# Kernel tuning notes

Measured on AMD Instinct MI355X. Metric: run time of the kernel, lower is better.

The kernel has to match this reference:

```python
import jax, jax.numpy as jnp
import numpy as np

B, T, D, H = 4, 8192, 512, 512


def log_g(x):
    # log of the 'continuous relu-ish' gate: log(relu(x)+0.5) for x>=0, -softplus(-x) otherwise
    return jnp.where(x >= 0, jnp.log(jax.nn.relu(x) + 0.5), -jax.nn.softplus(-x))


def setup_inputs() -> dict:
    key = jax.random.key(0)
    ks = jax.random.split(key, 8)
    s = 1.0 / np.sqrt(D)
    return {
        "x": jax.random.normal(ks[0], (B, T, D), dtype=jnp.float32),
        "h_0": jax.random.normal(ks[1], (B, 1, H), dtype=jnp.float32),
        "W_f": jax.random.normal(ks[2], (D, H), dtype=jnp.float32) * s,
        "b_f": jnp.zeros((H,), dtype=jnp.float32),
        "W_i": jax.random.normal(ks[3], (D, H), dtype=jnp.float32) * s,
        "b_i": jnp.zeros((H,), dtype=jnp.float32),
        "W_h": jax.random.normal(ks[4], (D, H), dtype=jnp.float32) * s,
        "b_h": jnp.zeros((H,), dtype=jnp.float32),
    }


def reference(x, h_0, W_f, b_f, W_i, b_i, W_h, b_h):
    # three dense gate projections: [B,T,H]
    f_pre = jnp.einsum("btd,dh->bth", x, W_f) + b_f
    i_pre = jnp.einsum("btd,dh->bth", x, W_i) + b_i
    h_pre = jnp.einsum("btd,dh->bth", x, W_h) + b_h

    diff = jax.nn.softplus(-f_pre) - jax.nn.softplus(-i_pre)
    log_f = -jax.nn.softplus(diff)            # log forget gate  [B,T,H]
    log_i = -jax.nn.softplus(-diff)           # log input  gate  [B,T,H]

    log_h0 = log_g(h_0)                       # [B,1,H]
    log_tilde_h = log_g(h_pre)                # [B,T,H]
    log_values = jnp.concatenate([log_h0, log_i + log_tilde_h], axis=1)  # [B,T+1,H]

    # a_star[t] = sum_{s<=t} log_f[s], with a leading zero for the h_0 slot
    a_star = jnp.pad(jnp.cumsum(log_f, axis=1), ((0, 0), (1, 0), (0, 0)))  # [B,T+1,H]
    # stable parallel scan in log space
    log_h = a_star + jax.lax.cumlogsumexp(log_values - a_star, axis=1)     # [B,T+1,H]
    return jnp.exp(log_h)
```

## Files before the change

### kernel.cpp

```cpp
#include <hip/hip_runtime.h>
#include <hip/hip_bf16.h>

#define B_ 4
#define T_ 8192
#define D_ 512
#define H_ 512
#define M_ (B_ * T_)
#define CHUNK_ 128
#define SUB_ 32
#define NSUB_ (T_ / SUB_)
#define SEQS_ (B_ * H_)

typedef __attribute__((ext_vector_type(8))) short bf16x8;
typedef __attribute__((ext_vector_type(4))) float f32x4;

__device__ __forceinline__ unsigned short f2bf(float x) {
  union { float f; unsigned int u; } c; c.f = x;
  unsigned int u = c.u;
  unsigned int r = (u + 0x7fffu + ((u >> 16) & 1u)) >> 16;
  return (unsigned short)r;
}
__device__ __forceinline__ float bf2f(unsigned short h) {
  union { unsigned int u; float f; } c; c.u = ((unsigned int)h) << 16;
  return c.f;
}

__device__ __forceinline__ void gll16(const void* g, void* l) {
  __builtin_amdgcn_global_load_lds(
      (const __attribute__((address_space(1))) unsigned int*)g,
      (__attribute__((address_space(3))) unsigned int*)l, 16, 0, 0);
}

__global__ void convert_all(const float* __restrict__ x, const float* __restrict__ Wf,
                            const float* __restrict__ Wi, const float* __restrict__ Wh,
                            unsigned short* __restrict__ xbf, unsigned short* __restrict__ Wt) {
  const int gid = blockIdx.x * 256 + threadIdx.x;
  const size_t i = (size_t)gid * 4;
  const float4 a = *(const float4*)(x + i);
  ushort4 hv;
  hv.x = f2bf(a.x); hv.y = f2bf(a.y); hv.z = f2bf(a.z); hv.w = f2bf(a.w);
  *(ushort4*)(xbf + i) = hv;
  if (gid < 3 * H_ * D_ / 4) {
    const int g = gid >> 16;
    const int rem = gid & 65535;
    const int n = rem >> 7;
    const int k4 = (rem & 127) * 4;
    const float* W = (g == 0) ? Wf : (g == 1) ? Wi : Wh;
    ushort4 o;
    o.x = f2bf(W[(k4 + 0) * H_ + n]);
    o.y = f2bf(W[(k4 + 1) * H_ + n]);
    o.z = f2bf(W[(k4 + 2) * H_ + n]);
    o.w = f2bf(W[(k4 + 3) * H_ + n]);
    *(ushort4*)(Wt + ((size_t)g * H_ + n) * D_ + k4) = o;
  }
}

__global__ __launch_bounds__(256, 2)
void gemm_gates(const unsigned short* __restrict__ xb, const unsigned short* __restrict__ Wt,
                const float* __restrict__ bF, const float* __restrict__ bI,
                const float* __restrict__ bH, unsigned int* __restrict__ AV) {
  __shared__ unsigned short xs[128 * 64];
  __shared__ unsigned short wsm[3 * 64 * 64];

  const int tid = threadIdx.x;
  const int hb = blockIdx.x;
  const int m0 = blockIdx.y * 128;
  const int n0 = hb * 64;
  const int wave = tid >> 6;
  const int lane = tid & 63;
  const int wm = (wave & 1) * 64;
  const int wn = (wave >> 1) * 32;
  const int l16 = lane & 15;
  const int quad = lane >> 4;
  const int lrow = lane >> 3;
  const int lch = (lane & 7) ^ lrow;

  int xoff[4];
  #pragma unroll
  for (int j = 0; j < 4; ++j)
    xoff[j] = (m0 + (wave * 4 + j) * 8 + lrow) * D_ + lch * 8;
  int woff[6], wdst[6];
  #pragma unroll
  for (int q = 0; q < 6; ++q) {
    const int gw = wave * 6 + q;
    const int g = gw >> 3, rg = gw & 7;
    woff[q] = (g * H_ + n0 + rg * 8 + lrow) * D_ + lch * 8;
    wdst[q] = g * 4096 + rg * 512;
  }

  f32x4 acc[3][4][2];
  #pragma unroll
  for (int g = 0; g < 3; ++g)
    #pragma unroll
    for (int mi = 0; mi < 4; ++mi)
      #pragma unroll
      for (int ni = 0; ni < 2; ++ni)
        acc[g][mi][ni] = (f32x4){0.f, 0.f, 0.f, 0.f};

  #pragma unroll 1
  for (int kb = 0; kb < D_; kb += 64) {
    #pragma unroll
    for (int j = 0; j < 4; ++j)
      gll16(xb + xoff[j] + kb, xs + (wave * 4 + j) * 512);
    #pragma unroll
    for (int q = 0; q < 6; ++q)
      gll16(Wt + woff[q] + kb, wsm + wdst[q]);
    __syncthreads();

    #pragma unroll
    for (int kk = 0; kk < 64; kk += 32) {
      const int kc = kk >> 3;
      bf16x8 af[4];
      #pragma unroll
      for (int mi = 0; mi < 4; ++mi) {
        const int r = wm + mi * 16 + l16;
        af[mi] = *(const bf16x8*)(xs + r * 64 + ((kc + quad) ^ (r & 7)) * 8);
      }
      bf16x8 bfr[3][2];
      #pragma unroll
      for (int g = 0; g < 3; ++g)
        #pragma unroll
        for (int ni = 0; ni < 2; ++ni) {
          const int r = wn + ni * 16 + l16;
          bfr[g][ni] = *(const bf16x8*)(wsm + g * 4096 + r * 64 + ((kc + quad) ^ (r & 7)) * 8);
        }
      #pragma unroll
      for (int g = 0; g < 3; ++g)
        #pragma unroll
        for (int mi = 0; mi < 4; ++mi)
          #pragma unroll
          for (int ni = 0; ni < 2; ++ni)
            acc[g][mi][ni] = __builtin_amdgcn_mfma_f32_16x16x32_bf16(
                af[mi], bfr[g][ni], acc[g][mi][ni], 0, 0, 0);
    }
    __syncthreads();
  }

  const size_t avbase = ((size_t)blockIdx.y * 8 + hb) * (CHUNK_ * 64);
  #pragma unroll
  for (int ni = 0; ni < 2; ++ni) {
    const int hl = wn + ni * 16 + l16;
    const int col = n0 + hl;
    const float bfv = bF[col], biv = bI[col], bhv = bH[col];
    #pragma unroll
    for (int mi = 0; mi < 4; ++mi) {
      const int tb = wm + mi * 16 + quad * 4;
      #pragma unroll
      for (int r = 0; r < 4; ++r) {
        float fp = acc[0][mi][ni][r] + bfv;
        float ip = acc[1][mi][ni][r] + biv;
        float hp = acc[2][mi][ni][r] + bhv;
        fp = fminf(fmaxf(fp, -30.f), 30.f);
        ip = fminf(fmaxf(ip, -30.f), 30.f);
        hp = fminf(fmaxf(hp, -30.f), 30.f);
        const float Ef = __expf(-fp);
        const float Ei = __expf(-ip);
        const float rr2 = 1.f / (2.f + Ef + Ei);
        const float fgate = (1.f + Ei) * rr2;
        const float igate = (1.f + Ef) * rr2;
        float gval;
        if (hp >= 0.f) gval = hp + 0.5f;
        else gval = 1.f / (1.f + __expf(-hp));
        const float vval = igate * gval;
        AV[avbase + (size_t)(tb + r) * 64 + hl] =
            (unsigned int)f2bf(fgate) | ((unsigned int)f2bf(vval) << 16);
      }
    }
  }
}

__global__ void scan_pass1(const unsigned int* __restrict__ AV,
                           float* __restrict__ Fc, float* __restrict__ Sc) {
  const int gid = blockIdx.x * 256 + threadIdx.x;
  const int hl = gid & 63;
  const int rest = gid >> 6;
  const int hbi = rest & 7;
  const int sub = (rest >> 3) & 3;
  const int c = (rest >> 5) & 63;
  const int b = rest >> 11;
  const unsigned int* p = AV + (size_t)((b * 64 + c) * 8 + hbi) * (CHUNK_ * 64)
                             + sub * SUB_ * 64 + hl;
  float F = 1.f, S = 0.f;
  #pragma unroll 8
  for (int t = 0; t < SUB_; ++t) {
    const unsigned int w = p[t * 64];
    const float a = bf2f((unsigned short)(w & 0xffffu));
    const float v = bf2f((unsigned short)(w >> 16));
    F *= a;
    S = fmaf(a, S, v);
  }
  const int sidx = c * 4 + sub;
  const int seq = b * 512 + hbi * 64 + hl;
  Fc[(size_t)sidx * SEQS_ + seq] = F;
  Sc[(size_t)sidx * SEQS_ + seq] = S;
}

__global__ __launch_bounds__(256, 2)
void scan_pass2(const float* __restrict__ h0, const float* __restrict__ Fc,
                const float* __restrict__ Sc, float* __restrict__ Hin,
                float* __restrict__ out) {
  __shared__ float Fs[NSUB_ * 32];
  __shared__ float Ss[NSUB_ * 32];
  __shared__ float Fg[8 * 32], Sg[8 * 32], Hg[8 * 32];

  const int tid = threadIdx.x;
  const int seq0 = blockIdx.x * 32;

  #pragma unroll 8
  for (int i = tid; i < NSUB_ * 32; i += 256) {
    const int sub = i >> 5;
    const int sl = i & 31;
    Fs[i] = Fc[(size_t)sub * SEQS_ + seq0 + sl];
    Ss[i] = Sc[(size_t)sub * SEQS_ + seq0 + sl];
  }
  __syncthreads();

  const int g = tid >> 5;
  const int sl = tid & 31;
  {
    float F = 1.f, S = 0.f;
    #pragma unroll 8
    for (int j = 0; j < 32; ++j) {
      const int idx = (g * 32 + j) * 32 + sl;
      S = fmaf(Fs[idx], S, Ss[idx]);
      F *= Fs[idx];
    }
    Fg[g * 32 + sl] = F;
    Sg[g * 32 + sl] = S;
  }
  __syncthreads();

  if (tid < 32) {
    const int seq = seq0 + tid;
    const int b = seq >> 9;
    const int h = seq & 511;
    const float xv = h0[seq];
    float hcur = (xv >= 0.f) ? (xv + 0.5f) : (1.f / (1.f + __expf(-xv)));
    out[(size_t)(b * (T_ + 1)) * H_ + h] = hcur;
    #pragma unroll
    for (int gg = 0; gg < 8; ++gg) {
      Hg[gg * 32 + tid] = hcur;
      hcur = fmaf(Fg[gg * 32 + tid], hcur, Sg[gg * 32 + tid]);
    }
  }
  __syncthreads();

  float h = Hg[g * 32 + sl];
  #pragma unroll 8
  for (int j = 0; j < 32; ++j) {
    const int sub = g * 32 + j;
    const int idx = sub * 32 + sl;
    Hin[(size_t)sub * SEQS_ + seq0 + sl] = h;
    h = fmaf(Fs[idx], h, Ss[idx]);
  }
}

__global__ void scan_pass3(const unsigned int* __restrict__ AV,
                           const float* __restrict__ Hin, float* __restrict__ out) {
  const int gid = blockIdx.x * 256 + threadIdx.x;
  const int hl = gid & 63;
  const int rest = gid >> 6;
  const int hbi = rest & 7;
  const int sub = (rest >> 3) & 3;
  const int c = (rest >> 5) & 63;
  const int b = rest >> 11;
  const unsigned int* p = AV + (size_t)((b * 64 + c) * 8 + hbi) * (CHUNK_ * 64)
                             + sub * SUB_ * 64 + hl;
  float* o = out + ((size_t)(b * (T_ + 1) + c * CHUNK_ + sub * SUB_ + 1) * H_)
                 + hbi * 64 + hl;
  const int seq = b * 512 + hbi * 64 + hl;
  float hcur = Hin[(size_t)(c * 4 + sub) * SEQS_ + seq];
  #pragma unroll 8
  for (int t = 0; t < SUB_; ++t) {
    const unsigned int w = p[t * 64];
    const float a = bf2f((unsigned short)(w & 0xffffu));
    const float v = bf2f((unsigned short)(w >> 16));
    hcur = fmaf(a, hcur, v);
    o[(size_t)t * H_] = hcur;
  }
}

extern "C" void kernel_launch(void* const* d_in, const int* in_sizes, int n_in,
                              void* d_out, int out_size, void* d_ws, size_t ws_size,
                              hipStream_t stream) {
  const float* x  = (const float*)d_in[0];
  const float* h0 = (const float*)d_in[1];
  const float* Wf = (const float*)d_in[2];
  const float* bF = (const float*)d_in[3];
  const float* Wi = (const float*)d_in[4];
  const float* bI = (const float*)d_in[5];
  const float* Wh = (const float*)d_in[6];
  const float* bH = (const float*)d_in[7];
  float* out = (float*)d_out;

  char* ws = (char*)d_ws;
  size_t off = 0;
  unsigned int* AV = (unsigned int*)(ws + off);      off += (size_t)M_ * H_ * 4;
  unsigned short* xbf = (unsigned short*)(ws + off); off += (size_t)M_ * D_ * 2;
  unsigned short* Wt = (unsigned short*)(ws + off);  off += (size_t)3 * H_ * D_ * 2;
  float* Fc  = (float*)(ws + off); off += (size_t)NSUB_ * SEQS_ * 4;
  float* Sc  = (float*)(ws + off); off += (size_t)NSUB_ * SEQS_ * 4;
  float* Hin = (float*)(ws + off); off += (size_t)NSUB_ * SEQS_ * 4;

  convert_all<<<(M_ * D_ / 4) / 256, 256, 0, stream>>>(x, Wf, Wi, Wh, xbf, Wt);
  gemm_gates<<<dim3(H_ / 64, M_ / 128), 256, 0, stream>>>(xbf, Wt, bF, bI, bH, AV);
  scan_pass1<<<(SEQS_ * NSUB_) / 256, 256, 0, stream>>>(AV, Fc, Sc);
  scan_pass2<<<SEQS_ / 32, 256, 0, stream>>>(h0, Fc, Sc, Hin, out);
  scan_pass3<<<(SEQS_ * NSUB_) / 256, 256, 0, stream>>>(AV, Hin, out);
}
```

Before: 229.8 us.

## Fuse scan pass1 sub-chunk reduction into GEMM epilogue and remap blocks per XCD

The per-32-step sub-chunk scan summaries (product of forget gates and accumulated value) are now computed in the GEMM epilogue from the rounded bf16 gate values. Each lane combines its 4 rows and merges across quads with xor-shuffles, which removes the separate scan_pass1 kernel and its full re-read of the AV buffer. The grid is also flattened to 1D and remapped so that the eight H-blocks sharing one M-chunk land on the same XCD, aiming for better L2 reuse of x tiles. The cost is extra epilogue work and register pressure in the GEMM.

```diff
diff --git a/kernel.cpp b/kernel.cpp
--- a/kernel.cpp
+++ b/kernel.cpp
@@ -58,14 +58,20 @@
 __global__ __launch_bounds__(256, 2)
 void gemm_gates(const unsigned short* __restrict__ xb, const unsigned short* __restrict__ Wt,
                 const float* __restrict__ bF, const float* __restrict__ bI,
-                const float* __restrict__ bH, unsigned int* __restrict__ AV) {
+                const float* __restrict__ bH, unsigned int* __restrict__ AV,
+                float* __restrict__ Fc, float* __restrict__ Sc) {
   __shared__ unsigned short xs[128 * 64];
   __shared__ unsigned short wsm[3 * 64 * 64];
 
   const int tid = threadIdx.x;
-  const int hb = blockIdx.x;
-  const int m0 = blockIdx.y * 128;
+  const int bid = blockIdx.x;
+  const int xcd = bid & 7;
+  const int kseq = bid >> 3;
+  const int mc = (kseq & ~7) | xcd;
+  const int hb = kseq & 7;
+  const int m0 = mc * CHUNK_;
   const int n0 = hb * 64;
+
   const int wave = tid >> 6;
   const int lane = tid & 63;
   const int wm = (wave & 1) * 64;
@@ -136,15 +142,18 @@
     __syncthreads();
   }
 
-  const size_t avbase = ((size_t)blockIdx.y * 8 + hb) * (CHUNK_ * 64);
+  const size_t avbase = ((size_t)mc * 8 + hb) * (CHUNK_ * 64);
+  const int bb = mc >> 6, cc = mc & 63;
   #pragma unroll
   for (int ni = 0; ni < 2; ++ni) {
     const int hl = wn + ni * 16 + l16;
     const int col = n0 + hl;
     const float bfv = bF[col], biv = bI[col], bhv = bH[col];
+    float Fseg[4], Sseg[4];
     #pragma unroll
     for (int mi = 0; mi < 4; ++mi) {
       const int tb = wm + mi * 16 + quad * 4;
+      float Fs_ = 1.f, Ss_ = 0.f;
       #pragma unroll
       for (int r = 0; r < 4; ++r) {
         float fp = acc[0][mi][ni][r] + bfv;
@@ -162,37 +171,42 @@
         if (hp >= 0.f) gval = hp + 0.5f;
         else gval = 1.f / (1.f + __expf(-hp));
         const float vval = igate * gval;
+        const unsigned short ab = f2bf(fgate);
+        const unsigned short vb = f2bf(vval);
         AV[avbase + (size_t)(tb + r) * 64 + hl] =
-            (unsigned int)f2bf(fgate) | ((unsigned int)f2bf(vval) << 16);
+            (unsigned int)ab | ((unsigned int)vb << 16);
+        const float ar = bf2f(ab), vr = bf2f(vb);
+        Ss_ = fmaf(ar, Ss_, vr);
+        Fs_ *= ar;
       }
-    }
-  }
-}
-
-__global__ void scan_pass1(const unsigned int* __restrict__ AV,
-                           float* __restrict__ Fc, float* __restrict__ Sc) {
-  const int gid = blockIdx.x * 256 + threadIdx.x;
-  const int hl = gid & 63;
-  const int rest = gid >> 6;
-  const int hbi = rest & 7;
-  const int sub = (rest >> 3) & 3;
-  const int c = (rest >> 5) & 63;
-  const int b = rest >> 11;
-  const unsigned int* p = AV + (size_t)((b * 64 + c) * 8 + hbi) * (CHUNK_ * 64)
-                             + sub * SUB_ * 64 + hl;
-  float F = 1.f, S = 0.f;
-  #pragma unroll 8
-  for (int t = 0; t < SUB_; ++t) {
-    const unsigned int w = p[t * 64];
-    const float a = bf2f((unsigned short)(w & 0xffffu));
-    const float v = bf2f((unsigned short)(w >> 16));
-    F *= a;
-    S = fmaf(a, S, v);
-  }
-  const int sidx = c * 4 + sub;
-  const int seq = b * 512 + hbi * 64 + hl;
-  Fc[(size_t)sidx * SEQS_ + seq] = F;
-  Sc[(size_t)sidx * SEQS_ + seq] = S;
+      Fseg[mi] = Fs_; Sseg[mi] = Ss_;
+    }
+    #pragma unroll
+    for (int mi = 0; mi < 4; ++mi) {
+      float F = Fseg[mi], S = Sseg[mi];
+      float Fo = __shfl_xor(F, 16);
+      float So = __shfl_xor(S, 16);
+      S = (quad & 1) ? fmaf(F, So, S) : fmaf(Fo, S, So);
+      F *= Fo;
+      Fo = __shfl_xor(F, 32);
+      So = __shfl_xor(S, 32);
+      S = (quad & 2) ? fmaf(F, So, S) : fmaf(Fo, S, So);
+      F *= Fo;
+      Fseg[mi] = F; Sseg[mi] = S;
+    }
+    if (quad == 0) {
+      #pragma unroll
+      for (int j = 0; j < 2; ++j) {
+        const float Fsub = Fseg[2 * j + 1] * Fseg[2 * j];
+        const float Ssub = fmaf(Fseg[2 * j + 1], Sseg[2 * j], Sseg[2 * j + 1]);
+        const int subl = (wave & 1) * 2 + j;
+        const int sidx = cc * 4 + subl;
+        const int seq = bb * 512 + hb * 64 + hl;
+        Fc[(size_t)sidx * SEQS_ + seq] = Fsub;
+        Sc[(size_t)sidx * SEQS_ + seq] = Ssub;
+      }
+    }
+  }
 }
 
 __global__ __launch_bounds__(256, 2)
@@ -303,8 +317,7 @@
   float* Hin = (float*)(ws + off); off += (size_t)NSUB_ * SEQS_ * 4;
 
   convert_all<<<(M_ * D_ / 4) / 256, 256, 0, stream>>>(x, Wf, Wi, Wh, xbf, Wt);
-  gemm_gates<<<dim3(H_ / 64, M_ / 128), 256, 0, stream>>>(xbf, Wt, bF, bI, bH, AV);
-  scan_pass1<<<(SEQS_ * NSUB_) / 256, 256, 0, stream>>>(AV, Fc, Sc);
+  gemm_gates<<<2048, 256, 0, stream>>>(xbf, Wt, bF, bI, bH, AV, Fc, Sc);
   scan_pass2<<<SEQS_ / 32, 256, 0, stream>>>(h0, Fc, Sc, Hin, out);
   scan_pass3<<<(SEQS_ * NSUB_) / 256, 256, 0, stream>>>(AV, Hin, out);
 }
```

Result: faster. 222.1 us (-3.3%).
